# Kernel optimization log

Hardware: AMD Instinct MI355X
Metric: run time of the kernel (lower is better)

The kernel has to match this reference:

```python
import jax, jax.numpy as jnp
import numpy as np

B, F, D, E = 16384, 2048, 256, 8  # batch, feature, expert out dim, n instrument experts (+1 default)


def setup_inputs() -> dict:
    key = jax.random.key(0)
    k1, k2, k3 = jax.random.split(key, 3)
    shared_features = jax.random.normal(k1, (B, F), dtype=jnp.float32)
    # instrument ids 0..E-1; id_to_index is the identity mapping here
    instrument_ids = jax.random.randint(k2, (B, 1), 0, E, dtype=jnp.int32)
    # stacked expert weights: E instrument layers + 1 default layer => E+1 Dense(F->D)
    W = jax.random.normal(k3, (E + 1, F, D), dtype=jnp.float32) * 0.02
    b = jnp.zeros((E + 1, D), dtype=jnp.float32)
    return {"shared_features": shared_features, "W": W, "b": b,
            "instrument_ids": instrument_ids}


def reference(shared_features, W, b, instrument_ids):
    # Compute ALL expert projections on the full batch (faithful to the TF layer),
    # stacked on axis=1: [B, E+1, D]
    stacked = jnp.einsum('bf,efd->bed', shared_features, W) + b
    # id_to_index lookup: ids are 0..E-1, identity mapping; default layer at index E unused
    idx = instrument_ids[:, 0].astype(jnp.int32)  # [B]
    # gather_nd equivalent: select per-sample expert output -> [B, D]
    selected = jnp.take_along_axis(stacked, idx[:, None, None], axis=1)[:, 0, :]
    return selected
```

## Files before the change

kernel.cpp:

```cpp
#include <hip/hip_runtime.h>
#include <hip/hip_bf16.h>

#define B_SZ 16384
#define F_SZ 2048
#define D_SZ 256
#define E_SZ 8
#define GRID_G 184
#define XCHUNK (GRID_G / 8)

typedef __attribute__((ext_vector_type(8))) short bhalf8;
typedef __attribute__((ext_vector_type(4))) float fl4;

__device__ __forceinline__ short f2b(float f) {
  __hip_bfloat16 h = __float2bfloat16(f);
  union { __hip_bfloat16 h; short s; } u;
  u.h = h;
  return u.s;
}

__global__ void k_scatter(const int* __restrict__ ids, int* __restrict__ counts,
                          int* __restrict__ perm) {
  __shared__ int lcnt[E_SZ], lbase[E_SZ];
  int t = threadIdx.x;
  if (t < E_SZ) lcnt[t] = 0;
  __syncthreads();
  int b = blockIdx.x * 256 + t;
  int e = ids[b];
  int p = atomicAdd(&lcnt[e], 1);
  __syncthreads();
  if (t < E_SZ) lbase[t] = atomicAdd(&counts[t], lcnt[t]);
  __syncthreads();
  perm[e * B_SZ + lbase[e] + p] = b;
}

__global__ void k_transpose(const float* __restrict__ W, __hip_bfloat16* __restrict__ Wt) {
  __shared__ float tile[64][65];
  int e = blockIdx.z;
  int f0 = blockIdx.x * 64;
  int d0 = blockIdx.y * 64;
  int t = threadIdx.x;
  const float* src = W + ((size_t)e * F_SZ + f0) * D_SZ + d0;
  int fr = t >> 2, c0 = t & 3;
#pragma unroll
  for (int c = c0; c < 16; c += 4) {
    float4 v = *(const float4*)(src + (size_t)fr * D_SZ + c * 4);
    tile[fr][c * 4 + 0] = v.x;
    tile[fr][c * 4 + 1] = v.y;
    tile[fr][c * 4 + 2] = v.z;
    tile[fr][c * 4 + 3] = v.w;
  }
  __syncthreads();
  int dr = t >> 2, cc = t & 3;
  union { unsigned short u[16]; bhalf8 v[2]; } pk;
#pragma unroll
  for (int k = 0; k < 16; ++k) pk.u[k] = (unsigned short)f2b(tile[cc * 16 + k][dr]);
  __hip_bfloat16* dst = Wt + ((size_t)e * D_SZ + d0 + dr) * F_SZ + f0 + cc * 16;
  ((bhalf8*)dst)[0] = pk.v[0];
  ((bhalf8*)dst)[1] = pk.v[1];
}

__device__ __forceinline__ void load_lds16(const __hip_bfloat16* g, __hip_bfloat16* l) {
  __builtin_amdgcn_global_load_lds((const __attribute__((address_space(1))) void*)g,
                                   (__attribute__((address_space(3))) void*)l, 16, 0, 0);
}

__launch_bounds__(512, 2)
__global__ void k_gemm(const float* __restrict__ x, const __hip_bfloat16* __restrict__ Wt,
                       const float* __restrict__ bias, const int* __restrict__ counts,
                       const int* __restrict__ perm, float* __restrict__ out) {
  int bid = blockIdx.x;
  int mt = (bid & 7) * XCHUNK + (bid >> 3);
  int e = -1, mbase = 0, count = 0;
  {
    int acc0 = 0;
#pragma unroll
    for (int ee = 0; ee < E_SZ; ++ee) {
      int c = counts[ee];
      int nt = (c + 95) / 96;
      if (e < 0 && mt < acc0 + nt) { e = ee; mbase = (mt - acc0) * 96; count = c; }
      acc0 += nt;
    }
  }
  if (e < 0) return;

  __shared__ __align__(16) __hip_bfloat16 As[2 * 96 * 64];
  __shared__ __align__(16) __hip_bfloat16 Bs[2 * 256 * 64];

  int t = threadIdx.x;
  int w = t >> 6;
  int lane = t & 63;
  int wm = w >> 2, wn = w & 3;
  int l15 = lane & 15;
  int q = lane >> 4;

  const int* permE = perm + e * B_SZ;

  int tr = t >> 4;
  int tc = t & 15;
  const float* pA[3];
  int wAo[3];
#pragma unroll
  for (int i = 0; i < 3; ++i) {
    int r = i * 32 + tr;
    int gm = mbase + r;
    int src = permE[(gm < count) ? gm : mbase];
    pA[i] = x + (size_t)src * F_SZ + tc * 4;
    int cw = tc >> 1, half = tc & 1;
    wAo[i] = r * 64 + ((cw ^ (r & 7)) * 8) + half * 4;
  }

  const __hip_bfloat16* pB[4];
  int dB[4];
#pragma unroll
  for (int i = 0; i < 4; ++i) {
    int p = i * 512 + t;
    int n = p >> 3;
    int cl = (p & 7) ^ (n & 7);
    pB[i] = Wt + (size_t)(e * D_SZ + n) * F_SZ + cl * 8;
    dB[i] = i * 4096 + w * 512;
  }

  int rAo[2][3], rBo[2][4];
#pragma unroll
  for (int ks = 0; ks < 2; ++ks) {
#pragma unroll
    for (int i = 0; i < 3; ++i) {
      int m = wm * 48 + i * 16 + l15;
      rAo[ks][i] = m * 64 + (((ks * 4 + q) ^ (m & 7)) * 8);
    }
#pragma unroll
    for (int j = 0; j < 4; ++j) {
      int n = wn * 64 + j * 16 + l15;
      rBo[ks][j] = n * 64 + (((ks * 4 + q) ^ (n & 7)) * 8);
    }
  }

  fl4 zz = {0.0f, 0.0f, 0.0f, 0.0f};
  fl4 acc[3][4];
#pragma unroll
  for (int i = 0; i < 3; ++i)
#pragma unroll
    for (int j = 0; j < 4; ++j) acc[i][j] = zz;

  float4 avA[3], avB[3];

#pragma unroll
  for (int i = 0; i < 4; ++i) load_lds16(pB[i], Bs + dB[i]);
  __builtin_amdgcn_sched_barrier(0);
  {
    float4 avP[3];
#pragma unroll
    for (int i = 0; i < 3; ++i) avP[i] = *(const float4*)(pA[i]);
#pragma unroll
    for (int i = 0; i < 3; ++i) {
      short4 s;
      s.x = f2b(avP[i].x); s.y = f2b(avP[i].y);
      s.z = f2b(avP[i].z); s.w = f2b(avP[i].w);
      *(short4*)(As + wAo[i]) = s;
    }
  }
#pragma unroll
  for (int i = 0; i < 3; ++i) avA[i] = *(const float4*)(pA[i] + 64);
#pragma unroll
  for (int i = 0; i < 3; ++i) avB[i] = *(const float4*)(pA[i] + 128);
  __builtin_amdgcn_sched_barrier(0);
  asm volatile("s_waitcnt vmcnt(6) lgkmcnt(0)");
  __builtin_amdgcn_sched_barrier(0);
  __builtin_amdgcn_s_barrier();
  __builtin_amdgcn_sched_barrier(0);

#define ITER(kk, AV)                                                                  \
  do {                                                                                \
    int cb_ = (kk) & 1, nx_ = cb_ ^ 1;                                                \
    _Pragma("unroll")                                                                 \
    for (int i = 0; i < 4; ++i)                                                       \
      load_lds16(pB[i] + ((kk) + 1) * 64, Bs + nx_ * 16384 + dB[i]);                  \
    __builtin_amdgcn_sched_barrier(0);                                                \
    _Pragma("unroll")                                                                 \
    for (int i = 0; i < 3; ++i) {                                                     \
      short4 s;                                                                       \
      s.x = f2b(AV[i].x); s.y = f2b(AV[i].y);                                         \
      s.z = f2b(AV[i].z); s.w = f2b(AV[i].w);                                         \
      *(short4*)(As + nx_ * 6144 + wAo[i]) = s;                                       \
    }                                                                                 \
    {                                                                                 \
      int kn_ = ((kk) + 3) & 31;                                                      \
      _Pragma("unroll")                                                               \
      for (int i = 0; i < 3; ++i) AV[i] = *(const float4*)(pA[i] + kn_ * 64);         \
    }                                                                                 \
    {                                                                                 \
      const __hip_bfloat16* Ab_ = As + cb_ * 6144;                                    \
      const __hip_bfloat16* Bb_ = Bs + cb_ * 16384;                                   \
      _Pragma("unroll")                                                               \
      for (int ks = 0; ks < 2; ++ks) {                                                \
        bhalf8 af[3], bf[4];                                                          \
        _Pragma("unroll")                                                             \
        for (int i = 0; i < 3; ++i) af[i] = *(const bhalf8*)(Ab_ + rAo[ks][i]);       \
        _Pragma("unroll")                                                             \
        for (int j = 0; j < 4; ++j) bf[j] = *(const bhalf8*)(Bb_ + rBo[ks][j]);       \
        _Pragma("unroll")                                                             \
        for (int i = 0; i < 3; ++i)                                                   \
          _Pragma("unroll")                                                           \
          for (int j = 0; j < 4; ++j)                                                 \
            acc[i][j] = __builtin_amdgcn_mfma_f32_16x16x32_bf16(af[i], bf[j],         \
                                                                acc[i][j], 0, 0, 0); \
      }                                                                               \
    }                                                                                 \
    __builtin_amdgcn_sched_barrier(0);                                                \
    asm volatile("s_waitcnt vmcnt(3) lgkmcnt(0)");                                    \
    __builtin_amdgcn_sched_barrier(0);                                                \
    __builtin_amdgcn_s_barrier();                                                     \
    __builtin_amdgcn_sched_barrier(0);                                                \
  } while (0)

  for (int k = 0; k < 30; k += 2) {
    ITER(k, avA);
    ITER(k + 1, avB);
  }
  ITER(30, avA);
#undef ITER

  asm volatile("" :: "v"(avA[0].x), "v"(avA[1].x), "v"(avA[2].x),
                     "v"(avB[0].x), "v"(avB[1].x), "v"(avB[2].x));

  {
    const __hip_bfloat16* Ab = As + 6144;
    const __hip_bfloat16* Bb = Bs + 16384;
#pragma unroll
    for (int ks = 0; ks < 2; ++ks) {
      bhalf8 af[3], bf[4];
#pragma unroll
      for (int i = 0; i < 3; ++i) af[i] = *(const bhalf8*)(Ab + rAo[ks][i]);
#pragma unroll
      for (int j = 0; j < 4; ++j) bf[j] = *(const bhalf8*)(Bb + rBo[ks][j]);
#pragma unroll
      for (int i = 0; i < 3; ++i)
#pragma unroll
        for (int j = 0; j < 4; ++j)
          acc[i][j] = __builtin_amdgcn_mfma_f32_16x16x32_bf16(af[i], bf[j], acc[i][j], 0, 0, 0);
    }
  }

  float bv[4];
#pragma unroll
  for (int j = 0; j < 4; ++j) bv[j] = bias[e * D_SZ + wn * 64 + j * 16 + l15];

#pragma unroll
  for (int i = 0; i < 3; ++i) {
#pragma unroll
    for (int r = 0; r < 4; ++r) {
      int gm = mbase + wm * 48 + i * 16 + q * 4 + r;
      if (gm < count) {
        int row = permE[gm];
        float* po = out + (size_t)row * D_SZ + wn * 64;
#pragma unroll
        for (int j = 0; j < 4; ++j) po[j * 16 + l15] = acc[i][j][r] + bv[j];
      }
    }
  }
}

extern "C" void kernel_launch(void* const* d_in, const int* in_sizes, int n_in,
                              void* d_out, int out_size, void* d_ws, size_t ws_size,
                              hipStream_t stream) {
  const float* x = (const float*)d_in[0];
  const float* W = (const float*)d_in[1];
  const float* bias = (const float*)d_in[2];
  const int* ids = (const int*)d_in[3];
  float* out = (float*)d_out;

  char* ws = (char*)d_ws;
  int* counts = (int*)ws;
  int* perm = (int*)(ws + 256);
  __hip_bfloat16* Wt = (__hip_bfloat16*)(ws + (1 << 20));

  hipMemsetAsync(counts, 0, E_SZ * sizeof(int), stream);
  k_scatter<<<B_SZ / 256, 256, 0, stream>>>(ids, counts, perm);
  k_transpose<<<dim3(F_SZ / 64, D_SZ / 64, E_SZ), 256, 0, stream>>>(W, Wt);
  k_gemm<<<GRID_G, 512, 0, stream>>>(x, Wt, bias, counts, perm, out);
}
```

Before: 236.3 us.

## Triple-buffer B tiles in LDS to prefetch two k-steps ahead

After: 236.9 us. Within noise of the previous version (+0.2%).

```diff
diff --git a/kernel.cpp b/kernel.cpp
--- a/kernel.cpp
+++ b/kernel.cpp
@@ -84,7 +84,7 @@
   if (e < 0) return;
 
   __shared__ __align__(16) __hip_bfloat16 As[2 * 96 * 64];
-  __shared__ __align__(16) __hip_bfloat16 Bs[2 * 256 * 64];
+  __shared__ __align__(16) __hip_bfloat16 Bs[3 * 256 * 64];
 
   int t = threadIdx.x;
   int w = t >> 6;
@@ -146,6 +146,8 @@
 
 #pragma unroll
   for (int i = 0; i < 4; ++i) load_lds16(pB[i], Bs + dB[i]);
+#pragma unroll
+  for (int i = 0; i < 4; ++i) load_lds16(pB[i] + 64, Bs + 16384 + dB[i]);
   __builtin_amdgcn_sched_barrier(0);
   {
     float4 avP[3];
@@ -169,19 +171,18 @@
   __builtin_amdgcn_s_barrier();
   __builtin_amdgcn_sched_barrier(0);
 
-#define ITER(kk, AV)                                                                  \
+#define ITER(kk, AV, MB, DB, MA, DA)                                                  \
   do {                                                                                \
-    int cb_ = (kk) & 1, nx_ = cb_ ^ 1;                                                \
     _Pragma("unroll")                                                                 \
     for (int i = 0; i < 4; ++i)                                                       \
-      load_lds16(pB[i] + ((kk) + 1) * 64, Bs + nx_ * 16384 + dB[i]);                  \
+      load_lds16(pB[i] + ((kk) + 2) * 64, Bs + (DB) * 16384 + dB[i]);                 \
     __builtin_amdgcn_sched_barrier(0);                                                \
     _Pragma("unroll")                                                                 \
     for (int i = 0; i < 3; ++i) {                                                     \
       short4 s;                                                                       \
       s.x = f2b(AV[i].x); s.y = f2b(AV[i].y);                                         \
       s.z = f2b(AV[i].z); s.w = f2b(AV[i].w);                                         \
-      *(short4*)(As + nx_ * 6144 + wAo[i]) = s;                                       \
+      *(short4*)(As + (DA) * 6144 + wAo[i]) = s;                                      \
     }                                                                                 \
     {                                                                                 \
       int kn_ = ((kk) + 3) & 31;                                                      \
@@ -189,8 +190,8 @@
       for (int i = 0; i < 3; ++i) AV[i] = *(const float4*)(pA[i] + kn_ * 64);         \
     }                                                                                 \
     {                                                                                 \
-      const __hip_bfloat16* Ab_ = As + cb_ * 6144;                                    \
-      const __hip_bfloat16* Bb_ = Bs + cb_ * 16384;                                   \
+      const __hip_bfloat16* Ab_ = As + (MA) * 6144;                                   \
+      const __hip_bfloat16* Bb_ = Bs + (MB) * 16384;                                  \
       _Pragma("unroll")                                                               \
       for (int ks = 0; ks < 2; ++ks) {                                                \
         bhalf8 af[3], bf[4];                                                          \
@@ -207,21 +208,52 @@
       }                                                                               \
     }                                                                                 \
     __builtin_amdgcn_sched_barrier(0);                                                \
-    asm volatile("s_waitcnt vmcnt(3) lgkmcnt(0)");                                    \
+    asm volatile("s_waitcnt vmcnt(10) lgkmcnt(0)");                                   \
     __builtin_amdgcn_sched_barrier(0);                                                \
     __builtin_amdgcn_s_barrier();                                                     \
     __builtin_amdgcn_sched_barrier(0);                                                \
   } while (0)
 
-  for (int k = 0; k < 30; k += 2) {
-    ITER(k, avA);
-    ITER(k + 1, avB);
-  }
-  ITER(30, avA);
+  for (int k = 0; k < 30; k += 6) {
+    ITER(k + 0, avA, 0, 2, 0, 1);
+    ITER(k + 1, avB, 1, 0, 1, 0);
+    ITER(k + 2, avA, 2, 1, 0, 1);
+    ITER(k + 3, avB, 0, 2, 1, 0);
+    ITER(k + 4, avA, 1, 0, 0, 1);
+    ITER(k + 5, avB, 2, 1, 1, 0);
+  }
 #undef ITER
 
-  asm volatile("" :: "v"(avA[0].x), "v"(avA[1].x), "v"(avA[2].x),
-                     "v"(avB[0].x), "v"(avB[1].x), "v"(avB[2].x));
+  {
+#pragma unroll
+    for (int i = 0; i < 3; ++i) {
+      short4 s;
+      s.x = f2b(avA[i].x); s.y = f2b(avA[i].y);
+      s.z = f2b(avA[i].z); s.w = f2b(avA[i].w);
+      *(short4*)(As + 6144 + wAo[i]) = s;
+    }
+    const __hip_bfloat16* Ab = As;
+    const __hip_bfloat16* Bb = Bs;
+#pragma unroll
+    for (int ks = 0; ks < 2; ++ks) {
+      bhalf8 af[3], bf[4];
+#pragma unroll
+      for (int i = 0; i < 3; ++i) af[i] = *(const bhalf8*)(Ab + rAo[ks][i]);
+#pragma unroll
+      for (int j = 0; j < 4; ++j) bf[j] = *(const bhalf8*)(Bb + rBo[ks][j]);
+#pragma unroll
+      for (int i = 0; i < 3; ++i)
+#pragma unroll
+        for (int j = 0; j < 4; ++j)
+          acc[i][j] = __builtin_amdgcn_mfma_f32_16x16x32_bf16(af[i], bf[j], acc[i][j], 0, 0, 0);
+    }
+  }
+  __builtin_amdgcn_sched_barrier(0);
+  asm volatile("s_waitcnt vmcnt(3) lgkmcnt(0)");
+  __builtin_amdgcn_sched_barrier(0);
+  __builtin_amdgcn_s_barrier();
+  __builtin_amdgcn_sched_barrier(0);
+  asm volatile("" :: "v"(avB[0].x), "v"(avB[1].x), "v"(avB[2].x));
 
   {
     const __hip_bfloat16* Ab = As + 6144;
```
